# Performance work log

Measured on AMD Instinct MI355X. Metric: run time of the kernel, lower is better.

## Reference

```python
import jax, jax.numpy as jnp
import numpy as np

PATCH_LEN = 16
PATCH_STRIDE = 8
DIM = 512
NUM_HEADS = 8
HEAD_DIM = DIM // NUM_HEADS
NUM_LAYERS = 4
MLP_HIDDEN = 4 * DIM
ROPE_BASE = 10000.0
LN_EPS = 1e-5


def setup_inputs() -> dict:
    key = jax.random.key(0)
    ks = jax.random.split(key, 20)
    B, T, C = 4, 8192, 7
    s = 0.02
    inp = {
        "x": jax.random.normal(ks[0], (B, T, C), dtype=jnp.float32),
        "W_emb": jax.random.normal(ks[1], (PATCH_LEN * C, DIM), dtype=jnp.float32) * s,
        "b_emb": jnp.zeros((DIM,), jnp.float32),
        "ln1_g": jnp.ones((NUM_LAYERS, DIM), jnp.float32),
        "ln1_b": jnp.zeros((NUM_LAYERS, DIM), jnp.float32),
        "W_qkv": jax.random.normal(ks[2], (NUM_LAYERS, DIM, 3 * DIM), dtype=jnp.float32) * s,
        "b_qkv": jnp.zeros((NUM_LAYERS, 3 * DIM), jnp.float32),
        "W_proj": jax.random.normal(ks[3], (NUM_LAYERS, DIM, DIM), dtype=jnp.float32) * s,
        "b_proj": jnp.zeros((NUM_LAYERS, DIM), jnp.float32),
        "ln2_g": jnp.ones((NUM_LAYERS, DIM), jnp.float32),
        "ln2_b": jnp.zeros((NUM_LAYERS, DIM), jnp.float32),
        "W_mlp1": jax.random.normal(ks[4], (NUM_LAYERS, DIM, MLP_HIDDEN), dtype=jnp.float32) * s,
        "b_mlp1": jnp.zeros((NUM_LAYERS, MLP_HIDDEN), jnp.float32),
        "W_mlp2": jax.random.normal(ks[5], (NUM_LAYERS, MLP_HIDDEN, DIM), dtype=jnp.float32) * s,
        "b_mlp2": jnp.zeros((NUM_LAYERS, DIM), jnp.float32),
        "lnf_g": jnp.ones((DIM,), jnp.float32),
        "lnf_b": jnp.zeros((DIM,), jnp.float32),
    }
    return inp


def _layer_norm(x, g, b):
    mu = jnp.mean(x, axis=-1, keepdims=True)
    var = jnp.mean(jnp.square(x - mu), axis=-1, keepdims=True)
    return (x - mu) * jax.lax.rsqrt(var + LN_EPS) * g + b


def _rotate_half(x):
    x1, x2 = jnp.split(x, 2, axis=-1)
    return jnp.concatenate((-x2, x1), axis=-1)


def _rope_cos_sin(seq_len):
    t = jnp.arange(seq_len, dtype=jnp.float32)
    inv_freq = 1.0 / (ROPE_BASE ** (jnp.arange(0, HEAD_DIM, 2, dtype=jnp.float32) / HEAD_DIM))
    freqs = jnp.outer(t, inv_freq)                      # [L, hd/2]
    emb = jnp.concatenate((freqs, freqs), axis=-1)      # [L, hd]
    return jnp.cos(emb), jnp.sin(emb)


def _forward(x, W_emb, b_emb, ln1_g, ln1_b, W_qkv, b_qkv, W_proj, b_proj,
             ln2_g, ln2_b, W_mlp1, b_mlp1, W_mlp2, b_mlp2, lnf_g, lnf_b):
    B, T, C = x.shape
    n = (T - PATCH_LEN) // PATCH_STRIDE + 1
    # torch unfold: [B, n, C, patch_len], then flattened as (C, patch_len)
    idx = jnp.arange(n)[:, None] * PATCH_STRIDE + jnp.arange(PATCH_LEN)[None, :]  # [n, P]
    patches = x[:, idx, :]                              # [B, n, P, C]
    patches = patches.transpose(0, 1, 3, 2).reshape(B, n, C * PATCH_LEN)
    emb = patches @ W_emb + b_emb                       # [B, n, D]

    cos, sin = _rope_cos_sin(n)                         # [n, hd]
    cos = cos[None, None, :, :]
    sin = sin[None, None, :, :]
    scale = HEAD_DIM ** -0.5

    h = emb
    for i in range(NUM_LAYERS):
        # --- attention ---
        y = _layer_norm(h, ln1_g[i], ln1_b[i])
        qkv = (y @ W_qkv[i] + b_qkv[i]).reshape(B, n, 3, NUM_HEADS, HEAD_DIM)
        qkv = qkv.transpose(2, 0, 3, 1, 4)              # [3, B, H, n, hd]
        q, k, v = qkv[0], qkv[1], qkv[2]
        q = q * cos + _rotate_half(q) * sin
        k = k * cos + _rotate_half(k) * sin
        attn = jax.nn.softmax(jnp.einsum('bhqd,bhkd->bhqk', q, k) * scale, axis=-1)
        o = jnp.einsum('bhqk,bhkd->bhqd', attn, v)      # [B, H, n, hd]
        o = o.transpose(0, 2, 1, 3).reshape(B, n, DIM)
        h = h + (o @ W_proj[i] + b_proj[i])
        # --- mlp ---
        y = _layer_norm(h, ln2_g[i], ln2_b[i])
        y = jax.nn.gelu(y @ W_mlp1[i] + b_mlp1[i], approximate=False)
        h = h + (y @ W_mlp2[i] + b_mlp2[i])

    x_out = _layer_norm(h, lnf_g, lnf_b)
    return emb, x_out


def reference(x, W_emb, b_emb, ln1_g, ln1_b, W_qkv, b_qkv, W_proj, b_proj,
              ln2_g, ln2_b, W_mlp1, b_mlp1, W_mlp2, b_mlp2, lnf_g, lnf_b):
    return _forward(x, W_emb, b_emb, ln1_g, ln1_b, W_qkv, b_qkv, W_proj, b_proj,
                    ln2_g, ln2_b, W_mlp1, b_mlp1, W_mlp2, b_mlp2, lnf_g, lnf_b)
```

## Files before the change

kernel.cpp:

```cpp
#include <hip/hip_runtime.h>
#include <hip/hip_bf16.h>
#include <math.h>

#define B_SZ 4
#define T_LEN 8192
#define C_IN 7
#define NPATCH 1023
#define DIM 512
#define NH 8
#define HD 64
#define NLAYERS 4
#define MLP_HID 2048
#define M_ROWS (B_SZ * NPATCH)
#define KEMB 128
#define LN_EPS 1e-5f

typedef __attribute__((ext_vector_type(8))) short short8;
typedef __attribute__((ext_vector_type(4))) float float4v;

static __device__ __forceinline__ unsigned short f2bf(float f) {
  __hip_bfloat16 h = __float2bfloat16(f);
  return *reinterpret_cast<unsigned short*>(&h);
}

static __device__ __forceinline__ void gload_lds16(const void* g, void* l) {
  __builtin_amdgcn_global_load_lds(
      (const __attribute__((address_space(1))) unsigned int*)g,
      (__attribute__((address_space(3))) unsigned int*)l, 16, 0, 0);
}

#define PB0 3072
#define PB1 4096
#define PB2 8192
#define PB3 12288
#define PB4 14334
#define PB5 14590
#define PB6 14718

__global__ __launch_bounds__(256) void prep_kernel(
    const float* __restrict__ W_qkv, unsigned short* __restrict__ wqkv_t,
    const float* __restrict__ W_proj, unsigned short* __restrict__ wproj_t,
    const float* __restrict__ W_mlp1, unsigned short* __restrict__ wmlp1_t,
    const float* __restrict__ W_mlp2, unsigned short* __restrict__ wmlp2_t,
    const float* __restrict__ x, unsigned short* __restrict__ Pm,
    const float* __restrict__ W_emb, unsigned short* __restrict__ Wembt,
    float2* __restrict__ rtab) {
  __shared__ float tile[32][33];
  const int bid = blockIdx.x, tid = threadIdx.x;

  auto do_wcvt = [&](const float* W, unsigned short* Wt, int K, int N,
                     int t, int nx, int ny) {
    int xb = t % nx, yb = (t / nx) % ny, L = t / (nx * ny);
    int n0 = xb * 32, k0 = yb * 32;
    const float* Ws = W + (size_t)L * K * N;
    unsigned short* Wd = Wt + (size_t)L * K * N;
    int tx = tid & 31, ty = tid >> 5;
    #pragma unroll
    for (int i = 0; i < 4; ++i)
      tile[ty + i * 8][tx] = Ws[(size_t)(k0 + ty + i * 8) * N + n0 + tx];
    __syncthreads();
    #pragma unroll
    for (int i = 0; i < 4; ++i)
      Wd[(size_t)(n0 + ty + i * 8) * K + k0 + tx] = f2bf(tile[tx][ty + i * 8]);
  };

  if (bid < PB0) {
    do_wcvt(W_qkv, wqkv_t, DIM, 3 * DIM, bid, 48, 16);
  } else if (bid < PB1) {
    do_wcvt(W_proj, wproj_t, DIM, DIM, bid - PB0, 16, 16);
  } else if (bid < PB2) {
    do_wcvt(W_mlp1, wmlp1_t, DIM, MLP_HID, bid - PB1, 64, 16);
  } else if (bid < PB3) {
    do_wcvt(W_mlp2, wmlp2_t, MLP_HID, DIM, bid - PB2, 16, 64);
  } else if (bid < PB4) {
    int idx = (bid - PB3) * 256 + tid;
    if (idx < M_ROWS * KEMB) {
      int row = idx >> 7, c = idx & 127;
      float v = 0.f;
      if (c < 112) {
        int b = row / NPATCH, i = row - b * NPATCH;
        int ci = c >> 4, p = c & 15;
        v = x[((size_t)b * T_LEN + (size_t)i * 8 + p) * C_IN + ci];
      }
      Pm[idx] = f2bf(v);
    }
  } else if (bid < PB5) {
    int idx = (bid - PB4) * 256 + tid;
    if (idx < DIM * KEMB) {
      int n = idx >> 7, k = idx & 127;
      float v = (k < 112) ? W_emb[(size_t)k * DIM + n] : 0.f;
      Wembt[idx] = f2bf(v);
    }
  } else {
    int idx = (bid - PB5) * 256 + tid;
    if (idx < NPATCH * 32) {
      int i = idx >> 5, j = idx & 31;
      float inv = powf(10000.0f, -(float)j * (1.0f / 32.0f));
      float sn, cs;
      sincosf((float)i * inv, &sn, &cs);
      rtab[idx] = make_float2(cs, sn);
    }
  }
}

template <bool BF>
__global__ __launch_bounds__(256) void ln_kernel(
    const float* __restrict__ in, const float* __restrict__ g,
    const float* __restrict__ bb, void* __restrict__ outv, int M) {
  int row = blockIdx.x * 4 + (threadIdx.x >> 6);
  if (row >= M) return;
  int lane = threadIdx.x & 63;
  const float* xr = in + (size_t)row * DIM;
  float v[8];
  float s = 0.f;
  #pragma unroll
  for (int k = 0; k < 8; ++k) { v[k] = xr[lane + 64 * k]; s += v[k]; }
  #pragma unroll
  for (int off = 32; off; off >>= 1) s += __shfl_down(s, off);
  s = __shfl(s, 0);
  float mu = s * (1.f / DIM);
  float q = 0.f;
  #pragma unroll
  for (int k = 0; k < 8; ++k) { float d = v[k] - mu; q = fmaf(d, d, q); }
  #pragma unroll
  for (int off = 32; off; off >>= 1) q += __shfl_down(q, off);
  q = __shfl(q, 0);
  float rstd = rsqrtf(q * (1.f / DIM) + LN_EPS);
  #pragma unroll
  for (int k = 0; k < 8; ++k) {
    int d = lane + 64 * k;
    float r = (v[k] - mu) * rstd * g[d] + bb[d];
    if (BF)
      ((unsigned short*)outv)[(size_t)row * DIM + d] = f2bf(r);
    else
      ((float*)outv)[(size_t)row * DIM + d] = r;
  }
}

template <int TM, int TN, int KSTEP, int EPI>
__global__ __launch_bounds__(256) void mfma_gemm(
    const unsigned short* __restrict__ A, const unsigned short* __restrict__ Bt,
    const float* __restrict__ bias, const float* __restrict__ res,
    float* __restrict__ Cf, float* __restrict__ Cf2,
    unsigned short* __restrict__ Cb, const float2* __restrict__ rtab,
    int M, int N, int K) {
  constexpr int WM = TM / 2, WN = TN / 2;
  constexpr int NI = WM / 16, NJ = WN / 16;
  constexpr int RCH = KSTEP / 8;
  constexpr int RPU = 64 / RCH;
  constexpr int AU = TM / RPU;
  constexpr int NU = (TM + TN) / RPU;
  constexpr int CPW = NU / 4;
  constexpr int SH = (KSTEP == 32) ? 1 : 0;
  __shared__ __align__(16) unsigned short As[2][TM][KSTEP];
  __shared__ __align__(16) unsigned short Bs[2][TN][KSTEP];
  const int bm = blockIdx.y * TM;
  const int bn = blockIdx.x * TN;
  const int tid = threadIdx.x;
  const int lane = tid & 63, wave = tid >> 6;
  const int quad = lane >> 4, l16 = lane & 15;
  const int wm = (wave & 1) * WM;
  const int wn = (wave >> 1) * WN;
  const int lrow = lane / RCH, lc = lane & (RCH - 1);
  const int rsw = (l16 >> SH) & (RCH - 1);

  float4v acc[NI][NJ];
  #pragma unroll
  for (int i = 0; i < NI; ++i)
    #pragma unroll
    for (int j = 0; j < NJ; ++j)
      acc[i][j] = (float4v){0.f, 0.f, 0.f, 0.f};

  auto stage = [&](int bufI, int kk) {
    #pragma unroll
    for (int it = 0; it < CPW; ++it) {
      int u = wave * CPW + it;
      if (u < AU) {
        int row = u * RPU + lrow;
        int col16 = lc ^ ((row >> SH) & (RCH - 1));
        gload_lds16(A + (size_t)(bm + row) * K + kk + col16 * 8,
                    &As[bufI][u * RPU][0]);
      } else {
        int row = (u - AU) * RPU + lrow;
        int col16 = lc ^ ((row >> SH) & (RCH - 1));
        gload_lds16(Bt + (size_t)(bn + row) * K + kk + col16 * 8,
                    &Bs[bufI][(u - AU) * RPU][0]);
      }
    }
  };

  stage(0, 0);
  int buf = 0;
  for (int k0 = 0; k0 < K; k0 += KSTEP, buf ^= 1) {
    __syncthreads();
    if (k0 + KSTEP < K) stage(buf ^ 1, k0 + KSTEP);
    #pragma unroll
    for (int t = 0; t < KSTEP / 32; ++t) {
      short8 af[NI], bfr[NJ];
      #pragma unroll
      for (int i = 0; i < NI; ++i) {
        int rslot = (t * 4 + quad) ^ rsw;
        af[i] = *(const short8*)&As[buf][wm + i * 16 + l16][rslot * 8];
      }
      #pragma unroll
      for (int j = 0; j < NJ; ++j) {
        int rslot = (t * 4 + quad) ^ rsw;
        bfr[j] = *(const short8*)&Bs[buf][wn + j * 16 + l16][rslot * 8];
      }
      __builtin_amdgcn_s_setprio(1);
      #pragma unroll
      for (int i = 0; i < NI; ++i)
        #pragma unroll
        for (int j = 0; j < NJ; ++j)
          acc[i][j] = __builtin_amdgcn_mfma_f32_16x16x32_bf16(
              af[i], bfr[j], acc[i][j], 0, 0, 0);
      __builtin_amdgcn_s_setprio(0);
    }
  }

  if (EPI == 6) {
    const int sec = (bn + wn) >> 9;
    #pragma unroll
    for (int i = 0; i < NI; ++i) {
      int gm0 = bm + wm + i * 16 + quad * 4;
      #pragma unroll
      for (int r = 0; r < 4; ++r) {
        int gm = gm0 + r;
        if (gm >= M) continue;
        size_t rowoff = (size_t)gm * N;
        if (sec < 2) {
          int ip = gm; if (ip >= 2046) ip -= 2046; if (ip >= 1023) ip -= 1023;
          float sc = (sec == 0) ? 0.125f : 1.f;
          #pragma unroll
          for (int j = 0; j < NJ / 2; ++j) {
            int gn = bn + wn + j * 16 + l16;
            float v0 = acc[i][j][r] + bias[gn];
            float v1 = acc[i][j + NJ / 2][r] + bias[gn + 32];
            float2 t = rtab[ip * 32 + j * 16 + l16];
            Cb[rowoff + gn]      = f2bf((v0 * t.x - v1 * t.y) * sc);
            Cb[rowoff + gn + 32] = f2bf((v1 * t.x + v0 * t.y) * sc);
          }
        } else {
          #pragma unroll
          for (int j = 0; j < NJ; ++j) {
            int gn = bn + wn + j * 16 + l16;
            Cb[rowoff + gn] = f2bf(acc[i][j][r] + bias[gn]);
          }
        }
      }
    }
    return;
  }

  #pragma unroll
  for (int j = 0; j < NJ; ++j) {
    int gn = bn + wn + j * 16 + l16;
    float bv = bias[gn];
    #pragma unroll
    for (int i = 0; i < NI; ++i) {
      int gm0 = bm + wm + i * 16 + quad * 4;
      #pragma unroll
      for (int r = 0; r < 4; ++r) {
        int gm = gm0 + r;
        if (gm < M) {
          float v = acc[i][j][r] + bv;
          size_t off = (size_t)gm * N + gn;
          if (EPI == 1) {
            Cf[off] = v + res[off];
          } else if (EPI == 2) {
            Cb[off] = f2bf(0.5f * v * (1.f + erff(v * 0.70710678118f)));
          } else if (EPI == 3) {
            Cb[off] = f2bf(v);
          } else {
            Cf[off] = v;
            Cf2[off] = v;
          }
        }
      }
    }
  }
}

#define APITCH 72

__global__ __launch_bounds__(512, 4) void attn_kernel(
    const unsigned short* __restrict__ qkvb, unsigned short* __restrict__ o) {
  const int bid = blockIdx.x;
  const int xcd = bid & 7, slot = bid >> 3;
  const int qt0 = (slot & 15) * 64;
  const int gh = xcd + 8 * (slot >> 4);
  const int h = gh & 7, b = gh >> 3;

  const int tid = threadIdx.x;
  const int lane = tid & 63, wave = tid >> 6;
  const int quad = lane >> 4, l16 = lane & 15;
  const int half = wave >> 2, wq = wave & 3;

  __shared__ __align__(16) unsigned short Ks[2][64][APITCH];
  __shared__ __align__(16) unsigned short Vt[2][64][APITCH];
  __shared__ __align__(16) unsigned short Ps[8][16][APITCH];

  short8 aq0 = {0, 0, 0, 0, 0, 0, 0, 0}, aq1 = aq0;
  {
    int qrow = qt0 + wq * 16 + l16;
    if (qrow < NPATCH) {
      const uint4* qr = (const uint4*)(qkvb + (size_t)(b * NPATCH + qrow) * (3 * DIM) + h * HD + quad * 8);
      aq0 = __builtin_bit_cast(short8, qr[0]);
      aq1 = __builtin_bit_cast(short8, qr[4]);
    }
  }

  const int krow = tid >> 2, kc0 = (tid & 3) * 16;
  const int kp2 = tid & 63, dg = tid >> 6;
  uint4 pk0, pk1, pv0, pv1;
  auto load_kv = [&](int js) {
    pk0 = pk1 = pv0 = pv1 = make_uint4(0u, 0u, 0u, 0u);
    int jk = js + krow;
    if (jk < NPATCH) {
      const unsigned short* kb = qkvb + (size_t)(b * NPATCH + jk) * (3 * DIM) + DIM + h * HD;
      pk0 = *(const uint4*)(kb + kc0);
      pk1 = *(const uint4*)(kb + kc0 + 8);
    }
    int jv = js + 2 * kp2;
    const unsigned short* vb = qkvb + (size_t)(b * NPATCH + jv) * (3 * DIM) + 2 * DIM + h * HD + dg * 8;
    if (jv < NPATCH)     pv0 = *(const uint4*)vb;
    if (jv + 1 < NPATCH) pv1 = *(const uint4*)(vb + 3 * DIM);
  };

  load_kv(0);

  float4v accO[4];
  #pragma unroll
  for (int j2 = 0; j2 < 4; ++j2) accO[j2] = (float4v){0.f, 0.f, 0.f, 0.f};
  float m_run[4] = {-1e30f, -1e30f, -1e30f, -1e30f};
  float lp[4] = {0.f, 0.f, 0.f, 0.f};

  constexpr int NIT = (NPATCH + 127) / 128;
  for (int it = 0; it < NIT; ++it) {
    if (it > 0) __syncthreads();
    {
      *(uint4*)&Ks[krow >> 6][krow & 63][kc0] = pk0;
      *(uint4*)&Ks[krow >> 6][krow & 63][kc0 + 8] = pk1;
      unsigned short va[8], vb8[8];
      *(uint4*)&va[0] = pv0;
      *(uint4*)&vb8[0] = pv1;
      const int vh = kp2 >> 5, lp2 = kp2 & 31;
      #pragma unroll
      for (int u = 0; u < 8; ++u) {
        unsigned pk = (unsigned)va[u] | ((unsigned)vb8[u] << 16);
        *(unsigned*)&Vt[vh][dg * 8 + u][2 * lp2] = pk;
      }
    }
    __syncthreads();
    if (it + 1 < NIT) load_kv((it + 1) * 128);

    const int j0 = it * 128 + half * 64;

    float4v s[4];
    __builtin_amdgcn_s_setprio(1);
    #pragma unroll
    for (int j = 0; j < 4; ++j) {
      s[j] = (float4v){0.f, 0.f, 0.f, 0.f};
      short8 bk0 = *(const short8*)&Ks[half][j * 16 + l16][quad * 8];
      short8 bk1 = *(const short8*)&Ks[half][j * 16 + l16][32 + quad * 8];
      s[j] = __builtin_amdgcn_mfma_f32_16x16x32_bf16(aq0, bk0, s[j], 0, 0, 0);
      s[j] = __builtin_amdgcn_mfma_f32_16x16x32_bf16(aq1, bk1, s[j], 0, 0, 0);
    }
    __builtin_amdgcn_s_setprio(0);

    float mx[4];
    #pragma unroll
    for (int r = 0; r < 4; ++r)
      mx[r] = fmaxf(fmaxf(s[0][r], s[1][r]), fmaxf(s[2][r], s[3][r]));
    #pragma unroll
    for (int mask = 1; mask < 16; mask <<= 1)
      #pragma unroll
      for (int r = 0; r < 4; ++r)
        mx[r] = fmaxf(mx[r], __shfl_xor(mx[r], mask));
    float gmax = fmaxf(fmaxf(mx[0] - m_run[0], mx[1] - m_run[1]),
                       fmaxf(mx[2] - m_run[2], mx[3] - m_run[3]));
    if (!__all(gmax <= 8.f)) {
      #pragma unroll
      for (int r = 0; r < 4; ++r) {
        float mnew = fmaxf(m_run[r], mx[r]);
        float al = __expf(m_run[r] - mnew);
        m_run[r] = mnew;
        lp[r] *= al;
        #pragma unroll
        for (int j2 = 0; j2 < 4; ++j2) accO[j2][r] *= al;
      }
    }
    #pragma unroll
    for (int j = 0; j < 4; ++j) {
      bool valid = (j0 + j * 16 + l16) < NPATCH;
      #pragma unroll
      for (int r = 0; r < 4; ++r) {
        float p = valid ? __expf(s[j][r] - m_run[r]) : 0.f;
        lp[r] += p;
        Ps[wave][quad * 4 + r][j * 16 + l16] = f2bf(p);
      }
    }

    short8 pa0 = *(const short8*)&Ps[wave][l16][quad * 8];
    short8 pa1 = *(const short8*)&Ps[wave][l16][32 + quad * 8];
    __builtin_amdgcn_s_setprio(1);
    #pragma unroll
    for (int j2 = 0; j2 < 4; ++j2) {
      short8 v0 = *(const short8*)&Vt[half][j2 * 16 + l16][quad * 8];
      short8 v1 = *(const short8*)&Vt[half][j2 * 16 + l16][32 + quad * 8];
      accO[j2] = __builtin_amdgcn_mfma_f32_16x16x32_bf16(pa0, v0, accO[j2], 0, 0, 0);
      accO[j2] = __builtin_amdgcn_mfma_f32_16x16x32_bf16(pa1, v1, accO[j2], 0, 0, 0);
    }
    __builtin_amdgcn_s_setprio(0);
  }

  #pragma unroll
  for (int mask = 1; mask < 16; mask <<= 1)
    #pragma unroll
    for (int r = 0; r < 4; ++r)
      lp[r] += __shfl_xor(lp[r], mask);

  float* Pf = (float*)&Ps[0][0][0];
  __syncthreads();
  if (half == 1) {
    #pragma unroll
    for (int j2 = 0; j2 < 4; ++j2)
      #pragma unroll
      for (int r = 0; r < 4; ++r)
        Pf[((wq * 64 + lane) << 4) + j2 * 4 + r] = accO[j2][r];
    if (l16 == 0) {
      #pragma unroll
      for (int r = 0; r < 4; ++r) {
        Pf[4096 + ((wq * 16 + quad * 4 + r) << 1)]     = m_run[r];
        Pf[4096 + ((wq * 16 + quad * 4 + r) << 1) + 1] = lp[r];
      }
    }
  }
  __syncthreads();
  if (half == 0) {
    #pragma unroll
    for (int r = 0; r < 4; ++r) {
      float m1 = Pf[4096 + ((wq * 16 + quad * 4 + r) << 1)];
      float l1 = Pf[4096 + ((wq * 16 + quad * 4 + r) << 1) + 1];
      float M = fmaxf(m_run[r], m1);
      float w0 = __expf(m_run[r] - M), w1 = __expf(m1 - M);
      float inv = 1.f / (w0 * lp[r] + w1 * l1);
      int qi = qt0 + wq * 16 + quad * 4 + r;
      if (qi < NPATCH) {
        size_t off = (size_t)(b * NPATCH + qi) * DIM + h * HD + l16;
        #pragma unroll
        for (int j2 = 0; j2 < 4; ++j2) {
          float a1 = Pf[((wq * 64 + lane) << 4) + j2 * 4 + r];
          o[off + j2 * 16] = f2bf((w0 * accO[j2][r] + w1 * a1) * inv);
        }
      }
    }
  }
}

extern "C" void kernel_launch(void* const* d_in, const int* in_sizes, int n_in,
                              void* d_out, int out_size, void* d_ws, size_t ws_size,
                              hipStream_t stream) {
  const float* x      = (const float*)d_in[0];
  const float* W_emb  = (const float*)d_in[1];
  const float* b_emb  = (const float*)d_in[2];
  const float* ln1_g  = (const float*)d_in[3];
  const float* ln1_b  = (const float*)d_in[4];
  const float* W_qkv  = (const float*)d_in[5];
  const float* b_qkv  = (const float*)d_in[6];
  const float* W_proj = (const float*)d_in[7];
  const float* b_proj = (const float*)d_in[8];
  const float* ln2_g  = (const float*)d_in[9];
  const float* ln2_b  = (const float*)d_in[10];
  const float* W_mlp1 = (const float*)d_in[11];
  const float* b_mlp1 = (const float*)d_in[12];
  const float* W_mlp2 = (const float*)d_in[13];
  const float* b_mlp2 = (const float*)d_in[14];
  const float* lnf_g  = (const float*)d_in[15];
  const float* lnf_b  = (const float*)d_in[16];
  float* out = (float*)d_out;

  float* h              = (float*)d_ws;
  unsigned short* qkvb  = (unsigned short*)(h + (size_t)M_ROWS * DIM);
  unsigned short* midbf = qkvb;
  unsigned short* ybf   = qkvb + (size_t)M_ROWS * MLP_HID;
  unsigned short* obf   = ybf;
  unsigned short* wqkv_t  = ybf + (size_t)M_ROWS * DIM;
  unsigned short* wproj_t = wqkv_t  + (size_t)NLAYERS * DIM * 3 * DIM;
  unsigned short* wmlp1_t = wproj_t + (size_t)NLAYERS * DIM * DIM;
  unsigned short* wmlp2_t = wmlp1_t + (size_t)NLAYERS * DIM * MLP_HID;
  float2* rtab = (float2*)(wmlp2_t + (size_t)NLAYERS * MLP_HID * DIM);
  unsigned short* Pm    = (unsigned short*)(rtab + (size_t)NPATCH * 32);
  unsigned short* Wembt = Pm + (size_t)M_ROWS * KEMB;

  prep_kernel<<<dim3(PB6), 256, 0, stream>>>(
      W_qkv, wqkv_t, W_proj, wproj_t, W_mlp1, wmlp1_t, W_mlp2, wmlp2_t,
      x, Pm, W_emb, Wembt, rtab);

  const int MT64 = (M_ROWS + 63) / 64;
  const int MT128 = (M_ROWS + 127) / 128;
  const int LNG = (M_ROWS + 3) / 4;

  mfma_gemm<64, 64, 64, 5><<<dim3(DIM / 64, MT64), 256, 0, stream>>>(
      Pm, Wembt, b_emb, nullptr, out, h, nullptr, nullptr, M_ROWS, DIM, KEMB);

  for (int L = 0; L < NLAYERS; ++L) {
    ln_kernel<true><<<LNG, 256, 0, stream>>>(h, ln1_g + L * DIM, ln1_b + L * DIM, ybf, M_ROWS);
    mfma_gemm<64, 128, 32, 6><<<dim3(3 * DIM / 128, MT64), 256, 0, stream>>>(
        ybf, wqkv_t + (size_t)L * DIM * 3 * DIM, b_qkv + L * 3 * DIM,
        nullptr, nullptr, nullptr, qkvb, rtab, M_ROWS, 3 * DIM, DIM);
    attn_kernel<<<dim3(512), 512, 0, stream>>>(qkvb, obf);
    mfma_gemm<64, 64, 64, 1><<<dim3(DIM / 64, MT64), 256, 0, stream>>>(
        obf, wproj_t + (size_t)L * DIM * DIM, b_proj + L * DIM,
        h, h, nullptr, nullptr, nullptr, M_ROWS, DIM, DIM);
    ln_kernel<true><<<LNG, 256, 0, stream>>>(h, ln2_g + L * DIM, ln2_b + L * DIM, ybf, M_ROWS);
    mfma_gemm<128, 128, 32, 2><<<dim3(MLP_HID / 128, MT128), 256, 0, stream>>>(
        ybf, wmlp1_t + (size_t)L * DIM * MLP_HID, b_mlp1 + L * MLP_HID,
        nullptr, nullptr, nullptr, midbf, nullptr, M_ROWS, MLP_HID, DIM);
    mfma_gemm<64, 64, 64, 1><<<dim3(DIM / 64, MT64), 256, 0, stream>>>(
        midbf, wmlp2_t + (size_t)L * MLP_HID * DIM, b_mlp2 + L * DIM,
        h, h, nullptr, nullptr, nullptr, M_ROWS, DIM, MLP_HID);
  }

  ln_kernel<false><<<LNG, 256, 0, stream>>>(h, lnf_g, lnf_b, out + (size_t)M_ROWS * DIM, M_ROWS);
}
```

Before: 612.3 us.

## Remap GEMM workgroups across XCDs, fold log2e into Q scale, widen QKV K-step

GEMM launches switch to a 1D grid, and block IDs are remapped so consecutive tiles stay on the same XCD (blockIdx & 7 striding), which should improve L2 reuse of A/B tiles. The attention softmax now uses exp2f, with log2(e) folded into the Q scaling in the QKV epilogue, and the lazy-rescale threshold is raised to match the base-2 domain. The QKV GEMM K-step goes from 32 to 64. The remap assumes the grid size is divisible by 8 and that M tiles times N tiles equals the grid size; with M_ROWS=4092 the 64-row tile count is exactly 64, so this holds.

Measured after the change: 582.2 us. 4.9% less time.

```diff
diff --git a/kernel.cpp b/kernel.cpp
--- a/kernel.cpp
+++ b/kernel.cpp
@@ -154,8 +154,11 @@
   constexpr int SH = (KSTEP == 32) ? 1 : 0;
   __shared__ __align__(16) unsigned short As[2][TM][KSTEP];
   __shared__ __align__(16) unsigned short Bs[2][TN][KSTEP];
-  const int bm = blockIdx.y * TM;
-  const int bn = blockIdx.x * TN;
+  const int nwg = gridDim.x;
+  const int nx = N / TN;
+  const int wg = (blockIdx.x & 7) * (nwg >> 3) + (blockIdx.x >> 3);
+  const int bm = (wg / nx) * TM;
+  const int bn = (wg % nx) * TN;
   const int tid = threadIdx.x;
   const int lane = tid & 63, wave = tid >> 6;
   const int quad = lane >> 4, l16 = lane & 15;
@@ -230,7 +233,7 @@
         size_t rowoff = (size_t)gm * N;
         if (sec < 2) {
           int ip = gm; if (ip >= 2046) ip -= 2046; if (ip >= 1023) ip -= 1023;
-          float sc = (sec == 0) ? 0.125f : 1.f;
+          float sc = (sec == 0) ? 0.125f * 1.44269504f : 1.f;
           #pragma unroll
           for (int j = 0; j < NJ / 2; ++j) {
             int gn = bn + wn + j * 16 + l16;
@@ -379,11 +382,11 @@
         mx[r] = fmaxf(mx[r], __shfl_xor(mx[r], mask));
     float gmax = fmaxf(fmaxf(mx[0] - m_run[0], mx[1] - m_run[1]),
                        fmaxf(mx[2] - m_run[2], mx[3] - m_run[3]));
-    if (!__all(gmax <= 8.f)) {
+    if (!__all(gmax <= 11.0f)) {
       #pragma unroll
       for (int r = 0; r < 4; ++r) {
         float mnew = fmaxf(m_run[r], mx[r]);
-        float al = __expf(m_run[r] - mnew);
+        float al = exp2f(m_run[r] - mnew);
         m_run[r] = mnew;
         lp[r] *= al;
         #pragma unroll
@@ -395,7 +398,7 @@
       bool valid = (j0 + j * 16 + l16) < NPATCH;
       #pragma unroll
       for (int r = 0; r < 4; ++r) {
-        float p = valid ? __expf(s[j][r] - m_run[r]) : 0.f;
+        float p = valid ? exp2f(s[j][r] - m_run[r]) : 0.f;
         lp[r] += p;
         Ps[wave][quad * 4 + r][j * 16 + l16] = f2bf(p);
       }
@@ -443,7 +446,7 @@
       float m1 = Pf[4096 + ((wq * 16 + quad * 4 + r) << 1)];
       float l1 = Pf[4096 + ((wq * 16 + quad * 4 + r) << 1) + 1];
       float M = fmaxf(m_run[r], m1);
-      float w0 = __expf(m_run[r] - M), w1 = __expf(m1 - M);
+      float w0 = exp2f(m_run[r] - M), w1 = exp2f(m1 - M);
       float inv = 1.f / (w0 * lp[r] + w1 * l1);
       int qi = qt0 + wq * 16 + quad * 4 + r;
       if (qi < NPATCH) {
@@ -497,27 +500,28 @@
       W_qkv, wqkv_t, W_proj, wproj_t, W_mlp1, wmlp1_t, W_mlp2, wmlp2_t,
       x, Pm, W_emb, Wembt, rtab);
 
-  const int MT64 = (M_ROWS + 63) / 64;
-  const int MT128 = (M_ROWS + 127) / 128;
   const int LNG = (M_ROWS + 3) / 4;
-
-  mfma_gemm<64, 64, 64, 5><<<dim3(DIM / 64, MT64), 256, 0, stream>>>(
+  const int G64x64  = (DIM / 64) * 64;
+  const int Gqkv    = (3 * DIM / 128) * 64;
+  const int Gmlp1   = (MLP_HID / 128) * 32;
+
+  mfma_gemm<64, 64, 64, 5><<<dim3(G64x64), 256, 0, stream>>>(
       Pm, Wembt, b_emb, nullptr, out, h, nullptr, nullptr, M_ROWS, DIM, KEMB);
 
   for (int L = 0; L < NLAYERS; ++L) {
     ln_kernel<true><<<LNG, 256, 0, stream>>>(h, ln1_g + L * DIM, ln1_b + L * DIM, ybf, M_ROWS);
-    mfma_gemm<64, 128, 32, 6><<<dim3(3 * DIM / 128, MT64), 256, 0, stream>>>(
+    mfma_gemm<64, 128, 64, 6><<<dim3(Gqkv), 256, 0, stream>>>(
         ybf, wqkv_t + (size_t)L * DIM * 3 * DIM, b_qkv + L * 3 * DIM,
         nullptr, nullptr, nullptr, qkvb, rtab, M_ROWS, 3 * DIM, DIM);
     attn_kernel<<<dim3(512), 512, 0, stream>>>(qkvb, obf);
-    mfma_gemm<64, 64, 64, 1><<<dim3(DIM / 64, MT64), 256, 0, stream>>>(
+    mfma_gemm<64, 64, 64, 1><<<dim3(G64x64), 256, 0, stream>>>(
         obf, wproj_t + (size_t)L * DIM * DIM, b_proj + L * DIM,
         h, h, nullptr, nullptr, nullptr, M_ROWS, DIM, DIM);
     ln_kernel<true><<<LNG, 256, 0, stream>>>(h, ln2_g + L * DIM, ln2_b + L * DIM, ybf, M_ROWS);
-    mfma_gemm<128, 128, 32, 2><<<dim3(MLP_HID / 128, MT128), 256, 0, stream>>>(
+    mfma_gemm<128, 128, 32, 2><<<dim3(Gmlp1), 256, 0, stream>>>(
         ybf, wmlp1_t + (size_t)L * DIM * MLP_HID, b_mlp1 + L * MLP_HID,
         nullptr, nullptr, nullptr, midbf, nullptr, M_ROWS, MLP_HID, DIM);
-    mfma_gemm<64, 64, 64, 1><<<dim3(DIM / 64, MT64), 256, 0, stream>>>(
+    mfma_gemm<64, 64, 64, 1><<<dim3(G64x64), 256, 0, stream>>>(
         midbf, wmlp2_t + (size_t)L * MLP_HID * DIM, b_mlp2 + L * DIM,
         h, h, nullptr, nullptr, nullptr, M_ROWS, DIM, MLP_HID);
   }
```
